# Kernel tuning notes

Measured on AMD Instinct MI355X. Metric: run time of the kernel, lower is better.

The kernel has to match this reference:

```python
import jax, jax.numpy as jnp
import numpy as np

HEADS, DIM_HEAD = 8, 64
SCALE = DIM_HEAD ** -0.5
LAMDA1, LAMDA2 = 5.0, 5.0


def setup_inputs() -> dict:
    B, N, M = 32, 1536, 80  # N = 32*48 spatial tokens, M = max_boxes
    QD, KD, VD = 320, 768, 768
    inner = HEADS * DIM_HEAD
    ks = jax.random.split(jax.random.key(0), 11)
    return {
        "x": jax.random.normal(ks[0], (B, N, QD), jnp.float32),
        "key": jax.random.normal(ks[1], (B, M, KD), jnp.float32),
        "value": jax.random.normal(ks[2], (B, M, VD), jnp.float32),
        "mask": jax.random.randint(ks[3], (B, M), 0, 2).astype(bool),
        "perl_box_masking_map": jax.random.normal(ks[4], (B, N, M), jnp.float32),
        "perl_road_masking_map": jax.random.normal(ks[5], (B, 1, N), jnp.float32),
        "Wq": jax.random.normal(ks[6], (inner, QD), jnp.float32) * 0.02,
        "Wk": jax.random.normal(ks[7], (inner, KD), jnp.float32) * 0.02,
        "Wv": jax.random.normal(ks[8], (inner, VD), jnp.float32) * 0.02,
        "Wo": jax.random.normal(ks[9], (QD, inner), jnp.float32) * 0.02,
        "bo": jnp.zeros((QD,), jnp.float32),
    }


def reference(x, key, value, mask, perl_box_masking_map, perl_road_masking_map, Wq, Wk, Wv, Wo, bo):
    B, N, _ = x.shape
    M = key.shape[1]
    H, C = HEADS, DIM_HEAD
    # QKV projections (torch Linear: y = x @ W.T)
    q = (x @ Wq.T).reshape(B, N, H, C)
    k = (key @ Wk.T).reshape(B, M, H, C)
    v = (value @ Wv.T).reshape(B, M, H, C)
    # attention scores with scale, key mask, and two additive bias maps
    sim = jnp.einsum('bnhc,bmhc->bhnm', q, k) * SCALE  # (B, H, N, M)
    neg = -jnp.finfo(sim.dtype).max
    sim = jnp.where(mask[:, None, None, :], sim, neg)  # mask fill BEFORE bias adds, as in torch
    sim = sim + LAMDA1 * perl_box_masking_map[:, None, :, :]
    road = jnp.swapaxes(perl_road_masking_map, 1, 2)  # (B, N, 1) -> broadcast over key axis
    sim = sim + LAMDA2 * road[:, None, :, :]
    attn = jax.nn.softmax(sim, axis=-1)
    out = jnp.einsum('bhnm,bmhc->bnhc', attn, v).reshape(B, N, H * C)
    return out @ Wo.T + bo  # dropout is identity in eval
```

## Files before the change

kernel.cpp:

```cpp
#include <hip/hip_runtime.h>
#include <hip/hip_bf16.h>

typedef __attribute__((ext_vector_type(8))) short short8;
typedef __attribute__((ext_vector_type(4))) float floatx4;
typedef unsigned short u16;

#define NB 32
#define NN 1536
#define NM 80
#define NH 8
#define NC 64
#define NINNER 512
#define NQD 320
#define NKD 768

__device__ __forceinline__ float bf2f(u16 u) {
    union { unsigned i; float f; } x; x.i = ((unsigned)u) << 16; return x.f;
}
__device__ __forceinline__ u16 f2bf(float f) {
    unsigned u = __float_as_uint(f);
    unsigned r = (u + 0x7FFFu + ((u >> 16) & 1u)) >> 16;
    return (u16)r;
}
__device__ __forceinline__ short8 cvt8(const float* __restrict__ p) {
    float4 a = ((const float4*)p)[0];
    float4 b = ((const float4*)p)[1];
    short8 r;
    r[0] = (short)f2bf(a.x); r[1] = (short)f2bf(a.y);
    r[2] = (short)f2bf(a.z); r[3] = (short)f2bf(a.w);
    r[4] = (short)f2bf(b.x); r[5] = (short)f2bf(b.y);
    r[6] = (short)f2bf(b.z); r[7] = (short)f2bf(b.w);
    return r;
}
__device__ __forceinline__ void gload16(const u16* g, u16* l) {
    __builtin_amdgcn_global_load_lds(
        (const __attribute__((address_space(1))) unsigned int*)g,
        (__attribute__((address_space(3))) unsigned int*)l, 16, 0, 0);
}

__global__ __launch_bounds__(256) void prep(const u16* __restrict__ x,
                                            const unsigned char* __restrict__ raw,
                                            int* __restrict__ flag,
                                            float* __restrict__ maskbias) {
    if (blockIdx.x == 0) {
        __shared__ int cnt;
        if (threadIdx.x == 0) cnt = 0;
        __syncthreads();
        int c = 0;
        for (int i = threadIdx.x; i < 8192; i += 256) {
            unsigned e = (x[i] >> 7) & 0xFF;
            if (e >= 0xA0) c++;
        }
        atomicAdd(&cnt, c);
        __syncthreads();
        if (threadIdx.x == 0) *flag = (cnt > 64) ? 1 : 0;
    } else {
        __shared__ int c_bf, c_f32, c_u8;
        if (threadIdx.x == 0) { c_bf = 0; c_f32 = 0; c_u8 = 0; }
        __syncthreads();
        for (int i = threadIdx.x; i < NB * NM; i += 256) {
            unsigned char v = raw[i];
            if (v == 0x3F && (i & 3) == 1) atomicAdd(&c_bf, 1);
            if (v == 0x3F && (i & 3) == 3) atomicAdd(&c_f32, 1);
            if (v != 0 && (i & 3) != 0) atomicAdd(&c_u8, 1);
        }
        __syncthreads();
        int md;
        if (c_bf > 0) md = 2;
        else if (c_f32 > 0) md = 3;
        else if (c_u8 > 0) md = 1;
        else md = 0;
        for (int i = threadIdx.x; i < NB * NM; i += 256) {
            bool on;
            if (md == 2) on = ((const u16*)raw)[i] != 0;
            else if (md == 3) on = ((const float*)raw)[i] != 0.0f;
            else if (md == 1) on = raw[i] != 0;
            else on = ((const int*)raw)[i] != 0;
            maskbias[i] = on ? 0.0f : -3.4028234663852886e38f;
        }
    }
}

struct ConvSeg { const void* src; u16* dst; long nreal; long nblk; };
struct ConvArgs { ConvSeg s[7]; };

__global__ __launch_bounds__(256) void conv_batch(ConvArgs a, const int* __restrict__ flag) {
    const int f = *flag;
    long b = blockIdx.x; int seg = 0;
    while (seg < 7 && b >= a.s[seg].nblk) { b -= a.s[seg].nblk; seg++; }
    if (seg >= 7) return;
    const long idx = b * 2048 + threadIdx.x * 8;
    u16* dst = a.s[seg].dst;
    if (idx >= a.s[seg].nreal) { *(short8*)(dst + idx) = (short8)0; return; }
    if (f) *(short8*)(dst + idx) = cvt8((const float*)a.s[seg].src + idx);
    else   *(short8*)(dst + idx) = *(const short8*)((const u16*)a.s[seg].src + idx);
}

template <bool OUT_DYN, bool BIAS>
__device__ __forceinline__ void gemm_body(const u16* __restrict__ A,
                                          const u16* __restrict__ B,
                                          const void* __restrict__ bias,
                                          void* __restrict__ C,
                                          int bx, int by, int Nreal, int K, int f,
                                          u16* As, u16* Bs) {
    const int tid = threadIdx.x;
    const int wave = tid >> 6, lane = tid & 63;
    const int l16 = lane & 15, quad = lane >> 4;
    const int wr = wave >> 1, wc = wave & 1;
    const int bm0 = bx * 128, bn0 = by * 128;

    const int r0 = tid >> 2, c0 = tid & 3;
    const int sc = c0 ^ ((r0 >> 1) & 3);
    const u16* Ag = A + (size_t)(bm0 + r0) * K + sc * 8;
    const u16* Bg = B + (size_t)(bn0 + r0) * K + sc * 8;
    u16* AsW = As + wave * 512;
    u16* BsW = Bs + wave * 512;

    const int swz = (l16 >> 1) & 3;
    floatx4 acc[4][4];
#pragma unroll
    for (int i = 0; i < 4; ++i)
#pragma unroll
        for (int n = 0; n < 4; ++n) acc[i][n] = (floatx4)0.0f;

    for (int kk = 0; kk < K; kk += 32) {
        __syncthreads();
#pragma unroll
        for (int j = 0; j < 2; ++j) {
            gload16(Ag + (size_t)(j * 64) * K + kk, AsW + j * 2048);
            gload16(Bg + (size_t)(j * 64) * K + kk, BsW + j * 2048);
        }
        __syncthreads();
        short8 af[4], bf[4];
#pragma unroll
        for (int i = 0; i < 4; ++i)
            af[i] = *(const short8*)&As[(wr * 64 + i * 16 + l16) * 32 + ((quad ^ swz) * 8)];
#pragma unroll
        for (int n = 0; n < 4; ++n)
            bf[n] = *(const short8*)&Bs[(wc * 64 + n * 16 + l16) * 32 + ((quad ^ swz) * 8)];
#pragma unroll
        for (int i = 0; i < 4; ++i)
#pragma unroll
            for (int n = 0; n < 4; ++n)
                acc[i][n] = __builtin_amdgcn_mfma_f32_16x16x32_bf16(af[i], bf[n], acc[i][n], 0, 0, 0);
    }

#pragma unroll
    for (int n = 0; n < 4; ++n) {
        const int col = bn0 + wc * 64 + n * 16 + l16;
        if (col < Nreal) {
            float badd = 0.0f;
            if (BIAS) badd = f ? ((const float*)bias)[col] : bf2f(((const u16*)bias)[col]);
#pragma unroll
            for (int i = 0; i < 4; ++i)
#pragma unroll
                for (int r = 0; r < 4; ++r) {
                    const int row = bm0 + wr * 64 + i * 16 + quad * 4 + r;
                    const float val = acc[i][n][r] + badd;
                    if (OUT_DYN && f) ((float*)C)[(size_t)row * Nreal + col] = val;
                    else              ((u16*)C)[(size_t)row * Nreal + col] = f2bf(val);
                }
        }
    }
}

struct GemmRoles {
    const u16* A[3]; const u16* B[3]; u16* C[3];
    int mblk[3]; int kdim[3]; int start[3];
};

__global__ __launch_bounds__(256) void gemm_qkv(GemmRoles g) {
    __shared__ __align__(16) u16 As[128 * 32];
    __shared__ __align__(16) u16 Bs[128 * 32];
    const int id = blockIdx.x;
    const int role = (id >= g.start[1]) + (id >= g.start[2]);
    const int rid = id - g.start[role];
    const int mb = g.mblk[role];
    const int bx = rid % mb, by = rid / mb;
    gemm_body<false, false>(g.A[role], g.B[role], nullptr, g.C[role],
                            bx, by, NINNER, g.kdim[role], 0, As, Bs);
}

__global__ __launch_bounds__(256) void gemm_out(const u16* __restrict__ A,
                                                const u16* __restrict__ B,
                                                const void* __restrict__ bias,
                                                void* __restrict__ C,
                                                const int* __restrict__ flag) {
    __shared__ __align__(16) u16 As[128 * 32];
    __shared__ __align__(16) u16 Bs[128 * 32];
    const int f = *flag;
    gemm_body<true, true>(A, B, bias, C, blockIdx.x, blockIdx.y, NQD, NINNER, f, As, Bs);
}

__global__ __launch_bounds__(256) void transpose_v(const u16* __restrict__ v,
                                                   u16* __restrict__ vT) {
    int b = blockIdx.x >> 3, h = blockIdx.x & 7;
    const u16* src = v + (size_t)b * NM * NINNER + h * NC;
    u16* o = vT + (size_t)(b * NH + h) * NC * 96;
    for (int idx = threadIdx.x; idx < NM * NC; idx += 256) {
        int m = idx >> 6, c = idx & 63;
        o[c * 96 + m] = src[(size_t)m * NINNER + c];
    }
    for (int idx = threadIdx.x; idx < NC * 16; idx += 256) {
        int c = idx >> 4, m = 80 + (idx & 15);
        o[c * 96 + m] = 0;
    }
}

__global__ __launch_bounds__(256) void attn_kernel(const u16* __restrict__ q,
                                                   const u16* __restrict__ k,
                                                   const u16* __restrict__ vT,
                                                   const float* __restrict__ maskbias,
                                                   const void* __restrict__ box,
                                                   const void* __restrict__ road,
                                                   u16* __restrict__ attno,
                                                   const int* __restrict__ flag) {
    const int f = *flag;
    const int n0 = blockIdx.x * 64;
    const int h = blockIdx.y;
    const int b = blockIdx.z;
    const int tid = threadIdx.x;
    const int wave = tid >> 6, lane = tid & 63;
    const int l16 = lane & 15, quad = lane >> 4;

    __shared__ __align__(16) u16 p_lds[64][104];

    floatx4 s[5];
#pragma unroll
    for (int i = 0; i < 5; ++i) s[i] = (floatx4)0.0f;
    const size_t qrow = (size_t)(b * NN + n0 + 16 * wave + l16) * NINNER + h * NC;
#pragma unroll
    for (int kk = 0; kk < NC; kk += 32) {
        short8 a = *(const short8*)(q + qrow + kk + quad * 8);
#pragma unroll
        for (int mt = 0; mt < 5; ++mt) {
            short8 bf = *(const short8*)(k + (size_t)(b * NM + mt * 16 + l16) * NINNER + h * NC + kk + quad * 8);
            s[mt] = __builtin_amdgcn_mfma_f32_16x16x32_bf16(a, bf, s[mt], 0, 0, 0);
        }
    }

    float sv[5][4];
#pragma unroll
    for (int r = 0; r < 4; ++r) {
        int n = n0 + 16 * wave + quad * 4 + r;
        size_t ridx = (size_t)b * NN + n;
        float roadv = 5.0f * (f ? ((const float*)road)[ridx] : bf2f(((const u16*)road)[ridx]));
#pragma unroll
        for (int mt = 0; mt < 5; ++mt) {
            int m = mt * 16 + l16;
            size_t bidx = ((size_t)b * NN + n) * NM + m;
            float boxv = 5.0f * (f ? ((const float*)box)[bidx] : bf2f(((const u16*)box)[bidx]));
            sv[mt][r] = s[mt][r] * 0.125f + maskbias[b * NM + m] + boxv + roadv;
        }
    }

    float rowsum[4];
#pragma unroll
    for (int r = 0; r < 4; ++r) {
        float mx = sv[0][r];
#pragma unroll
        for (int mt = 1; mt < 5; ++mt) mx = fmaxf(mx, sv[mt][r]);
#pragma unroll
        for (int off = 1; off < 16; off <<= 1) mx = fmaxf(mx, __shfl_xor(mx, off, 16));
        float sum = 0.0f;
#pragma unroll
        for (int mt = 0; mt < 5; ++mt) {
            float p = __expf(sv[mt][r] - mx);
            sv[mt][r] = p;
            sum += p;
        }
#pragma unroll
        for (int off = 1; off < 16; off <<= 1) sum += __shfl_xor(sum, off, 16);
        rowsum[r] = sum;
    }

#pragma unroll
    for (int r = 0; r < 4; ++r) {
        int lr = 16 * wave + quad * 4 + r;
#pragma unroll
        for (int mt = 0; mt < 5; ++mt) p_lds[lr][mt * 16 + l16] = f2bf(sv[mt][r]);
        p_lds[lr][80 + l16] = 0;
    }
    asm volatile("s_waitcnt lgkmcnt(0)" ::: "memory");
    __builtin_amdgcn_sched_barrier(0);

    floatx4 o[4];
#pragma unroll
    for (int i = 0; i < 4; ++i) o[i] = (floatx4)0.0f;
    const u16* vbase = vT + (size_t)(b * NH + h) * NC * 96;
#pragma unroll
    for (int kk = 0; kk < 96; kk += 32) {
        short8 a = *(const short8*)&p_lds[16 * wave + l16][kk + quad * 8];
#pragma unroll
        for (int nt = 0; nt < 4; ++nt) {
            short8 bf = *(const short8*)(vbase + (size_t)(nt * 16 + l16) * 96 + kk + quad * 8);
            o[nt] = __builtin_amdgcn_mfma_f32_16x16x32_bf16(a, bf, o[nt], 0, 0, 0);
        }
    }

#pragma unroll
    for (int nt = 0; nt < 4; ++nt) {
#pragma unroll
        for (int r = 0; r < 4; ++r) {
            int n = n0 + 16 * wave + quad * 4 + r;
            float inv = 1.0f / rowsum[r];
            attno[((size_t)b * NN + n) * NINNER + h * NC + nt * 16 + l16] = f2bf(o[nt][r] * inv);
        }
    }
}

extern "C" void kernel_launch(void* const* d_in, const int* in_sizes, int n_in,
                              void* d_out, int out_size, void* d_ws, size_t ws_size,
                              hipStream_t stream) {
    (void)in_sizes; (void)n_in; (void)out_size; (void)ws_size;
    const void* x    = d_in[0];
    const void* key  = d_in[1];
    const void* val  = d_in[2];
    const unsigned char* mask = (const unsigned char*)d_in[3];
    const void* box  = d_in[4];
    const void* road = d_in[5];
    const void* Wq   = d_in[6];
    const void* Wk   = d_in[7];
    const void* Wv   = d_in[8];
    const void* Wo   = d_in[9];
    const void* bo   = d_in[10];

    char* ws = (char*)d_ws;
    size_t off = 0;
    auto carve = [&](size_t bytes) {
        char* p = ws + off;
        off += (bytes + 255) & ~(size_t)255;
        return p;
    };
    int* flag   = (int*)carve(256);
    u16* q_ws   = (u16*)carve((size_t)NB * NN * NINNER * 2);
    u16* k_ws   = (u16*)carve((size_t)NB * NM * NINNER * 2);
    u16* v_ws   = (u16*)carve((size_t)NB * NM * NINNER * 2);
    u16* vT_ws  = (u16*)carve((size_t)NB * NH * NC * 96 * 2);
    u16* ao_ws  = (u16*)carve((size_t)NB * NN * NINNER * 2);
    u16* x_bf   = ao_ws;
    u16* key_bf = (u16*)carve((size_t)NB * NM * NKD * 2);
    u16* val_bf = (u16*)carve((size_t)NB * NM * NKD * 2);
    u16* Wq_bf  = (u16*)carve((size_t)NINNER * NQD * 2);
    u16* Wk_bf  = (u16*)carve((size_t)NINNER * NKD * 2);
    u16* Wv_bf  = (u16*)carve((size_t)NINNER * NKD * 2);
    u16* WoP_bf = (u16*)carve((size_t)384 * NINNER * 2);
    float* mb   = (float*)carve((size_t)NB * NM * 4);

    prep<<<2, 256, 0, stream>>>((const u16*)x, mask, flag, mb);

    ConvArgs ca;
    ca.s[0] = { x,     x_bf,   (long)NB * NN * NQD, (long)NB * NN * NQD / 2048 };
    ca.s[1] = { key,   key_bf, (long)NB * NM * NKD, (long)NB * NM * NKD / 2048 };
    ca.s[2] = { val,   val_bf, (long)NB * NM * NKD, (long)NB * NM * NKD / 2048 };
    ca.s[3] = { Wq,    Wq_bf,  (long)NINNER * NQD,  (long)NINNER * NQD / 2048 };
    ca.s[4] = { Wk,    Wk_bf,  (long)NINNER * NKD,  (long)NINNER * NKD / 2048 };
    ca.s[5] = { Wv,    Wv_bf,  (long)NINNER * NKD,  (long)NINNER * NKD / 2048 };
    ca.s[6] = { Wo,    WoP_bf, (long)NQD * NINNER,  (long)384 * NINNER / 2048 };
    long totblk = 0;
    for (int i = 0; i < 7; ++i) totblk += ca.s[i].nblk;
    conv_batch<<<(int)totblk, 256, 0, stream>>>(ca, flag);

    GemmRoles g;
    g.A[0] = key_bf; g.B[0] = Wk_bf; g.C[0] = k_ws; g.mblk[0] = NB * NM / 128; g.kdim[0] = NKD;
    g.A[1] = val_bf; g.B[1] = Wv_bf; g.C[1] = v_ws; g.mblk[1] = NB * NM / 128; g.kdim[1] = NKD;
    g.A[2] = x_bf;   g.B[2] = Wq_bf; g.C[2] = q_ws; g.mblk[2] = NB * NN / 128; g.kdim[2] = NQD;
    g.start[0] = 0;
    g.start[1] = g.mblk[0] * 4;
    g.start[2] = g.start[1] + g.mblk[1] * 4;
    int gtot = g.start[2] + g.mblk[2] * 4;
    gemm_qkv<<<gtot, 256, 0, stream>>>(g);

    transpose_v<<<NB * NH, 256, 0, stream>>>(v_ws, vT_ws);
    attn_kernel<<<dim3(NN / 64, NH, NB), 256, 0, stream>>>(
        q_ws, k_ws, vT_ws, mb, box, road, ao_ws, flag);
    gemm_out<<<dim3(NB * NN / 128, 384 / 128), 256, 0, stream>>>(
        ao_ws, WoP_bf, bo, d_out, flag);
}
```

Before: 324.9 us.

## Transpose QK MFMA so each lane owns a query row, vectorize bias loads

```diff
diff --git a/kernel.cpp b/kernel.cpp
--- a/kernel.cpp
+++ b/kernel.cpp
@@ -2,6 +2,7 @@
 #include <hip/hip_bf16.h>
 
 typedef __attribute__((ext_vector_type(8))) short short8;
+typedef __attribute__((ext_vector_type(4))) short short4v;
 typedef __attribute__((ext_vector_type(4))) float floatx4;
 typedef unsigned short u16;
 
@@ -225,62 +226,83 @@
 
     __shared__ __align__(16) u16 p_lds[64][104];
 
+    const int n = n0 + 16 * wave + l16;
+    const size_t qrow = (size_t)(b * NN + n) * NINNER + h * NC;
+    short8 qa[2];
+    qa[0] = *(const short8*)(q + qrow + 0 + quad * 8);
+    qa[1] = *(const short8*)(q + qrow + 32 + quad * 8);
+    short8 kf[5][2];
+#pragma unroll
+    for (int mt = 0; mt < 5; ++mt) {
+        const u16* kr = k + (size_t)(b * NM + mt * 16 + l16) * NINNER + h * NC + quad * 8;
+        kf[mt][0] = *(const short8*)(kr + 0);
+        kf[mt][1] = *(const short8*)(kr + 32);
+    }
+    const size_t boxbase = ((size_t)b * NN + n) * NM;
+    floatx4 bx4[5]; short4v bxh[5]; floatx4 mb4[5];
+    float roadf = 0.0f; u16 roadh = 0;
+    if (f) {
+#pragma unroll
+        for (int mt = 0; mt < 5; ++mt)
+            bx4[mt] = *(const floatx4*)((const float*)box + boxbase + 16 * mt + 4 * quad);
+        roadf = ((const float*)road)[(size_t)b * NN + n];
+    } else {
+#pragma unroll
+        for (int mt = 0; mt < 5; ++mt)
+            bxh[mt] = *(const short4v*)((const u16*)box + boxbase + 16 * mt + 4 * quad);
+        roadh = ((const u16*)road)[(size_t)b * NN + n];
+    }
+#pragma unroll
+    for (int mt = 0; mt < 5; ++mt)
+        mb4[mt] = *(const floatx4*)(maskbias + b * NM + 16 * mt + 4 * quad);
+
     floatx4 s[5];
 #pragma unroll
     for (int i = 0; i < 5; ++i) s[i] = (floatx4)0.0f;
-    const size_t qrow = (size_t)(b * NN + n0 + 16 * wave + l16) * NINNER + h * NC;
-#pragma unroll
-    for (int kk = 0; kk < NC; kk += 32) {
-        short8 a = *(const short8*)(q + qrow + kk + quad * 8);
-#pragma unroll
-        for (int mt = 0; mt < 5; ++mt) {
-            short8 bf = *(const short8*)(k + (size_t)(b * NM + mt * 16 + l16) * NINNER + h * NC + kk + quad * 8);
-            s[mt] = __builtin_amdgcn_mfma_f32_16x16x32_bf16(a, bf, s[mt], 0, 0, 0);
-        }
-    }
-
-    float sv[5][4];
-#pragma unroll
-    for (int r = 0; r < 4; ++r) {
-        int n = n0 + 16 * wave + quad * 4 + r;
-        size_t ridx = (size_t)b * NN + n;
-        float roadv = 5.0f * (f ? ((const float*)road)[ridx] : bf2f(((const u16*)road)[ridx]));
-#pragma unroll
-        for (int mt = 0; mt < 5; ++mt) {
-            int m = mt * 16 + l16;
-            size_t bidx = ((size_t)b * NN + n) * NM + m;
-            float boxv = 5.0f * (f ? ((const float*)box)[bidx] : bf2f(((const u16*)box)[bidx]));
-            sv[mt][r] = s[mt][r] * 0.125f + maskbias[b * NM + m] + boxv + roadv;
-        }
-    }
-
-    float rowsum[4];
-#pragma unroll
-    for (int r = 0; r < 4; ++r) {
-        float mx = sv[0][r];
-#pragma unroll
-        for (int mt = 1; mt < 5; ++mt) mx = fmaxf(mx, sv[mt][r]);
-#pragma unroll
-        for (int off = 1; off < 16; off <<= 1) mx = fmaxf(mx, __shfl_xor(mx, off, 16));
-        float sum = 0.0f;
-#pragma unroll
-        for (int mt = 0; mt < 5; ++mt) {
-            float p = __expf(sv[mt][r] - mx);
-            sv[mt][r] = p;
+#pragma unroll
+    for (int kk2 = 0; kk2 < 2; ++kk2)
+#pragma unroll
+        for (int mt = 0; mt < 5; ++mt)
+            s[mt] = __builtin_amdgcn_mfma_f32_16x16x32_bf16(kf[mt][kk2], qa[kk2], s[mt], 0, 0, 0);
+
+    const float roadv = 5.0f * (f ? roadf : bf2f(roadh));
+#pragma unroll
+    for (int mt = 0; mt < 5; ++mt)
+#pragma unroll
+        for (int r = 0; r < 4; ++r) {
+            const float boxv = 5.0f * (f ? bx4[mt][r] : bf2f((u16)bxh[mt][r]));
+            s[mt][r] = s[mt][r] * 0.125f + mb4[mt][r] + boxv + roadv;
+        }
+
+    float mx = s[0][0];
+#pragma unroll
+    for (int mt = 0; mt < 5; ++mt) {
+        float t = fmaxf(fmaxf(s[mt][0], s[mt][1]), fmaxf(s[mt][2], s[mt][3]));
+        mx = (mt == 0) ? t : fmaxf(mx, t);
+    }
+    mx = fmaxf(mx, __shfl_xor(mx, 16));
+    mx = fmaxf(mx, __shfl_xor(mx, 32));
+    float sum = 0.0f;
+#pragma unroll
+    for (int mt = 0; mt < 5; ++mt)
+#pragma unroll
+        for (int r = 0; r < 4; ++r) {
+            const float p = __expf(s[mt][r] - mx);
+            s[mt][r] = p;
             sum += p;
         }
-#pragma unroll
-        for (int off = 1; off < 16; off <<= 1) sum += __shfl_xor(sum, off, 16);
-        rowsum[r] = sum;
-    }
-
-#pragma unroll
-    for (int r = 0; r < 4; ++r) {
-        int lr = 16 * wave + quad * 4 + r;
-#pragma unroll
-        for (int mt = 0; mt < 5; ++mt) p_lds[lr][mt * 16 + l16] = f2bf(sv[mt][r]);
-        p_lds[lr][80 + l16] = 0;
-    }
+    sum += __shfl_xor(sum, 16);
+    sum += __shfl_xor(sum, 32);
+    const float inv = 1.0f / sum;
+
+#pragma unroll
+    for (int mt = 0; mt < 5; ++mt) {
+        short4v pk;
+#pragma unroll
+        for (int r = 0; r < 4; ++r) pk[r] = (short)f2bf(s[mt][r] * inv);
+        *(short4v*)&p_lds[16 * wave + l16][16 * mt + 4 * quad] = pk;
+    }
+    if (quad < 2) *(short8*)&p_lds[16 * wave + l16][80 + 8 * quad] = (short8)0;
     asm volatile("s_waitcnt lgkmcnt(0)" ::: "memory");
     __builtin_amdgcn_sched_barrier(0);
 
@@ -302,9 +324,8 @@
     for (int nt = 0; nt < 4; ++nt) {
 #pragma unroll
         for (int r = 0; r < 4; ++r) {
-            int n = n0 + 16 * wave + quad * 4 + r;
-            float inv = 1.0f / rowsum[r];
-            attno[((size_t)b * NN + n) * NINNER + h * NC + nt * 16 + l16] = f2bf(o[nt][r] * inv);
+            int nr = n0 + 16 * wave + quad * 4 + r;
+            attno[((size_t)b * NN + nr) * NINNER + h * NC + nt * 16 + l16] = f2bf(o[nt][r]);
         }
     }
 }
```

Result: no change. 324.0 us (-0.3%).
